# Kernel optimization log

Measured on AMD Instinct MI355X. Metric: run time of the kernel, lower is better.

The kernel has to match this reference:

```python
import jax, jax.numpy as jnp
import numpy as np

N_NODES = 50000
BN_EPS = 1e-5


def _gin_layer(x, src, dst, W1, b1, gamma, beta, W2, b2):
    # GINConv (eps=0): h = MLP(x + sum_{j->i} x_j)
    agg = jax.ops.segment_sum(x[src], dst, num_segments=N_NODES)  # [N, F]
    h = (x + agg) @ W1 + b1                                       # [N, H]
    # BatchNorm1d over node dim (training-mode batch statistics, biased var)
    mean = jnp.mean(h, axis=0)
    var = jnp.mean((h - mean) ** 2, axis=0)
    h = (h - mean) * jax.lax.rsqrt(var + BN_EPS) * gamma + beta
    h = jax.nn.relu(h)
    h = jax.nn.relu(h @ W2 + b2)
    return h


def setup_inputs() -> dict:
    key = jax.random.key(0)
    ks = jax.random.split(key, 16)
    F_in, H = 9, 256
    E = 800000
    x = jax.random.normal(ks[0], (N_NODES, F_in), dtype=jnp.float32)
    edge_index = jax.random.randint(ks[1], (2, E), 0, N_NODES, dtype=jnp.int64)

    def lin(k, fi, fo):
        s = 1.0 / np.sqrt(fi)
        kw, kb = jax.random.split(k)
        W = jax.random.uniform(kw, (fi, fo), jnp.float32, -s, s)
        b = jax.random.uniform(kb, (fo,), jnp.float32, -s, s)
        return W, b

    inp = {"x": x, "edge_index": edge_index}
    dims = [(F_in, H), (H, H), (H, H)]
    for i, (fi, fo) in enumerate(dims, start=1):
        W1, b1 = lin(ks[2 * i], fi, fo)
        W2, b2 = lin(ks[2 * i + 1], fo, fo)
        inp[f"W1_{i}"] = W1; inp[f"b1_{i}"] = b1
        inp[f"g_{i}"] = jnp.ones((fo,), jnp.float32)
        inp[f"be_{i}"] = jnp.zeros((fo,), jnp.float32)
        inp[f"W2_{i}"] = W2; inp[f"b2_{i}"] = b2
    return inp


def reference(x, edge_index,
              W1_1, b1_1, g_1, be_1, W2_1, b2_1,
              W1_2, b1_2, g_2, be_2, W2_2, b2_2,
              W1_3, b1_3, g_3, be_3, W2_3, b2_3):
    src, dst = edge_index[0], edge_index[1]
    h = _gin_layer(x, src, dst, W1_1, b1_1, g_1, be_1, W2_1, b2_1)
    h = jax.nn.relu(h)
    h = _gin_layer(h, src, dst, W1_2, b1_2, g_2, be_2, W2_2, b2_2)
    h = jax.nn.relu(h)
    h = _gin_layer(h, src, dst, W1_3, b1_3, g_3, be_3, W2_3, b2_3)
    h = jax.nn.relu(h)
    return jnp.sum(h, axis=0)  # [256]
```

## Files before the change

kernel.cpp:

```cpp
#include <hip/hip_runtime.h>

#define NN 50000
#define NE 800000
#define HD 256
#define BN_EPS 1e-5f

typedef __attribute__((ext_vector_type(8))) short bf16x8;
typedef __attribute__((ext_vector_type(8))) unsigned short ushort8;
typedef __attribute__((ext_vector_type(4))) float f32x4;

__device__ __forceinline__ float bf2f(unsigned short u) {
  union { unsigned int i; float f; } c; c.i = ((unsigned int)u) << 16; return c.f;
}
__device__ __forceinline__ unsigned short f2bf(float x) {
  union { float f; unsigned int i; } c; c.f = x;
  unsigned int r = (c.i + 0x7fffu + ((c.i >> 16) & 1u)) >> 16;
  return (unsigned short)r;
}

__global__ __launch_bounds__(1024) void k_zero(int* __restrict__ cursor, float* __restrict__ s_sum,
                                               float* __restrict__ s_sq, float* __restrict__ out) {
  int i = blockIdx.x * 1024 + threadIdx.x;
  if (i < NN) cursor[i] = 0;
  if (i < HD) { s_sum[i] = 0.f; s_sq[i] = 0.f; out[i] = 0.f; }
}

__global__ __launch_bounds__(256) void k_count(const int* __restrict__ dst, int* __restrict__ cnt) {
  int e = blockIdx.x * 256 + threadIdx.x;
  if (e < NE) atomicAdd(&cnt[dst[e]], 1);
}

__global__ __launch_bounds__(1024) void k_scan_a(const int* __restrict__ cnt,
                                                 int* __restrict__ rp, int* __restrict__ bsum) {
  __shared__ int wsum[16];
  int i = blockIdx.x * 1024 + threadIdx.x;
  int v = (i < NN) ? cnt[i] : 0;
  int lane = threadIdx.x & 63, wid = threadIdx.x >> 6;
  int s = v;
  #pragma unroll
  for (int off = 1; off < 64; off <<= 1) {
    int tv = __shfl_up(s, off);
    if (lane >= off) s += tv;
  }
  if (lane == 63) wsum[wid] = s;
  __syncthreads();
  if (wid == 0) {
    int ws = (lane < 16) ? wsum[lane] : 0;
    #pragma unroll
    for (int off = 1; off < 16; off <<= 1) {
      int tv = __shfl_up(ws, off);
      if (lane >= off) ws += tv;
    }
    if (lane < 16) wsum[lane] = ws;
  }
  __syncthreads();
  int excl = s - v + (wid > 0 ? wsum[wid - 1] : 0);
  if (i < NN) rp[i] = excl;
  if (threadIdx.x == 1023) bsum[blockIdx.x] = excl + v;
}

__global__ __launch_bounds__(1024) void k_scan_b(const int* __restrict__ bsum,
                                                 int* __restrict__ rp, int* __restrict__ cursor) {
  __shared__ int off_s;
  if (threadIdx.x < 64) {
    int v = ((int)threadIdx.x < (int)blockIdx.x && threadIdx.x < 49) ? bsum[threadIdx.x] : 0;
    #pragma unroll
    for (int o = 32; o > 0; o >>= 1) v += __shfl_xor(v, o);
    if (threadIdx.x == 0) off_s = v;
  }
  __syncthreads();
  int i = blockIdx.x * 1024 + threadIdx.x;
  if (i < NN) {
    int r = rp[i] + off_s;
    rp[i] = r;
    cursor[i] = r;
  }
  if (blockIdx.x == 0 && threadIdx.x == 0) rp[NN] = NE;
}

__global__ __launch_bounds__(256) void k_fill(const int* __restrict__ src, const int* __restrict__ dst,
                                              int* __restrict__ cursor, int* __restrict__ col) {
  int e = blockIdx.x * 256 + threadIdx.x;
  if (e < NE) {
    int p = atomicAdd(&cursor[dst[e]], 1);
    col[p] = src[e];
  }
}

__global__ __launch_bounds__(256) void k_prepW5(const float* __restrict__ Wa, const float* __restrict__ Wb,
    const float* __restrict__ Wc, const float* __restrict__ Wd, const float* __restrict__ We,
    unsigned short* __restrict__ out) {
  const float* W = (blockIdx.y == 0) ? Wa : (blockIdx.y == 1) ? Wb : (blockIdx.y == 2) ? Wc
                   : (blockIdx.y == 3) ? Wd : We;
  unsigned short* O = out + (size_t)blockIdx.y * HD * HD;
  int k = blockIdx.x, n = threadIdx.x;
  int nt = n >> 4, ks = k >> 5, lane = ((k >> 3) & 3) * 16 + (n & 15), j = k & 7;
  O[(size_t)((nt * 8 + ks) * 64 + lane) * 8 + j] = f2bf(W[k * 256 + n]);
}

__global__ __launch_bounds__(256) void k_agg9(const float* __restrict__ x,
    const int* __restrict__ rp, const int* __restrict__ col, float* __restrict__ u) {
  int i = blockIdx.x * 256 + threadIdx.x;
  if (i >= NN) return;
  float a[9];
  #pragma unroll
  for (int k = 0; k < 9; ++k) a[k] = x[(size_t)i * 9 + k];
  int e1 = rp[i + 1];
  for (int e = rp[i]; e < e1; ++e) {
    int nb = col[e];
    #pragma unroll
    for (int k = 0; k < 9; ++k) a[k] += x[(size_t)nb * 9 + k];
  }
  #pragma unroll
  for (int k = 0; k < 9; ++k) u[(size_t)i * 16 + k] = a[k];
}

__global__ __launch_bounds__(256) void k_l1gemm(const float* __restrict__ u,
    const float* __restrict__ W1, const float* __restrict__ b1,
    unsigned short* __restrict__ h, float* __restrict__ s_sum, float* __restrict__ s_sq) {
  __shared__ float Ws[9][256];
  int t = threadIdx.x;
  #pragma unroll
  for (int k = 0; k < 9; ++k) Ws[k][t] = W1[k * 256 + t];
  float bj = b1[t];
  __syncthreads();
  int r0 = blockIdx.x * 128;
  int r1 = min(r0 + 128, NN);
  float sum = 0.f, sq = 0.f;
  for (int r = r0; r < r1; ++r) {
    float acc = bj;
    #pragma unroll
    for (int k = 0; k < 9; ++k) acc = fmaf(u[(size_t)r * 16 + k], Ws[k][t], acc);
    h[(size_t)r * 256 + t] = f2bf(acc);
    sum += acc; sq += acc * acc;
  }
  atomicAdd(&s_sum[t], sum);
  atomicAdd(&s_sq[t], sq);
}

__global__ void k_finalize(float* __restrict__ s_sum, float* __restrict__ s_sq,
                           const float* __restrict__ g, const float* __restrict__ be,
                           float* __restrict__ scale, float* __restrict__ shift) {
  int j = threadIdx.x;
  float m = s_sum[j] / (float)NN;
  float v = s_sq[j] / (float)NN - m * m;
  v = fmaxf(v, 0.f);
  float sc = rsqrtf(v + BN_EPS) * g[j];
  scale[j] = sc;
  shift[j] = be[j] - m * sc;
  s_sum[j] = 0.f;
  s_sq[j] = 0.f;
}

__global__ __launch_bounds__(256) void k_bnapply(const unsigned short* __restrict__ h,
    const float* __restrict__ scale, const float* __restrict__ shift, unsigned short* __restrict__ a) {
  __shared__ float sc[256], sh[256];
  sc[threadIdx.x] = scale[threadIdx.x];
  sh[threadIdx.x] = shift[threadIdx.x];
  __syncthreads();
  const int total = NN * 32;
  for (int idx = blockIdx.x * 256 + threadIdx.x; idx < total; idx += gridDim.x * 256) {
    int c0 = (idx & 31) * 8;
    ushort8 v = *(const ushort8*)(h + (size_t)idx * 8);
    ushort8 o;
    #pragma unroll
    for (int j = 0; j < 8; ++j) {
      float f = bf2f(v[j]);
      f = fmaxf(fmaf(f, sc[c0 + j], sh[c0 + j]), 0.f);
      o[j] = f2bf(f);
    }
    *(ushort8*)(a + (size_t)idx * 8) = o;
  }
}

__global__ __launch_bounds__(256) void k_agg256(const unsigned short* __restrict__ f,
    const int* __restrict__ rp, const int* __restrict__ col, unsigned short* __restrict__ u) {
  int half = threadIdx.x >> 5;
  int lane32 = threadIdx.x & 31;
  int node = blockIdx.x * 8 + threadIdx.y * 2 + half;
  if (node >= NN) return;
  float acc[8];
  ushort8 v = *(const ushort8*)(f + (size_t)node * HD + lane32 * 8);
  #pragma unroll
  for (int j = 0; j < 8; ++j) acc[j] = bf2f(v[j]);
  int e0 = rp[node], e1 = rp[node + 1];
  int e = e0;
  for (; e + 1 < e1; e += 2) {
    int nb0 = col[e], nb1 = col[e + 1];
    ushort8 w0 = *(const ushort8*)(f + (size_t)nb0 * HD + lane32 * 8);
    ushort8 w1 = *(const ushort8*)(f + (size_t)nb1 * HD + lane32 * 8);
    #pragma unroll
    for (int j = 0; j < 8; ++j) acc[j] += bf2f(w0[j]) + bf2f(w1[j]);
  }
  if (e < e1) {
    int nb = col[e];
    ushort8 w = *(const ushort8*)(f + (size_t)nb * HD + lane32 * 8);
    #pragma unroll
    for (int j = 0; j < 8; ++j) acc[j] += bf2f(w[j]);
  }
  ushort8 o;
  #pragma unroll
  for (int j = 0; j < 8; ++j) o[j] = f2bf(acc[j]);
  *(ushort8*)(u + (size_t)node * HD + lane32 * 8) = o;
}

template<bool STATS, bool RELU, bool OUTSUM, bool WRITE>
__global__ __launch_bounds__(256, 3) void k_mfma_gemm(
    const unsigned short* __restrict__ A, const unsigned short* __restrict__ Bp,
    const float* __restrict__ bias, unsigned short* __restrict__ C,
    float* __restrict__ s_sum, float* __restrict__ s_sq, float* __restrict__ out)
{
  __shared__ unsigned short As[2][64 * 64];
  const int t = threadIdx.x;
  const int w = t >> 6;
  const int lane = t & 63;
  const int brow = blockIdx.x * 64;
  const bf16x8* Bf = (const bf16x8*)Bp;

  f32x4 zero; zero.x = zero.y = zero.z = zero.w = 0.f;
  f32x4 acc[4][4];
  #pragma unroll
  for (int i = 0; i < 4; ++i)
    #pragma unroll
    for (int j = 0; j < 4; ++j) acc[i][j] = zero;

  auto stage = [&](int buf, int kt) {
    #pragma unroll
    for (int hh = 0; hh < 2; ++hh) {
      int r0 = w * 16 + hh * 8;
      int row = r0 + (lane >> 3);
      int gp = (lane & 7) ^ (row & 7);
      int grow = brow + row; if (grow >= NN) grow = NN - 1;
      const unsigned short* gptr = A + (size_t)grow * HD + kt + gp * 8;
      __builtin_amdgcn_global_load_lds(
          (const __attribute__((address_space(1))) void*)gptr,
          (__attribute__((address_space(3))) void*)&As[buf][r0 * 64], 16, 0, 0);
    }
  };

  bf16x8 bcur[4], bnxt[4];
  #pragma unroll
  for (int ntl = 0; ntl < 4; ++ntl)
    bcur[ntl] = Bf[(size_t)((w * 4 + ntl) * 8 + 0) * 64 + lane];
  stage(0, 0);
  __syncthreads();

  #pragma unroll
  for (int step = 0; step < 8; ++step) {
    const int tt = step >> 1, s = step & 1;
    if (s == 0 && tt < 3) stage((tt + 1) & 1, (tt + 1) * 64);
    if (step < 7) {
      #pragma unroll
      for (int ntl = 0; ntl < 4; ++ntl)
        bnxt[ntl] = Bf[(size_t)((w * 4 + ntl) * 8 + step + 1) * 64 + lane];
    }
    bf16x8 afr[4];
    #pragma unroll
    for (int mt = 0; mt < 4; ++mt) {
      int row = mt * 16 + (lane & 15);
      int g = s * 4 + (lane >> 4);
      int gp = g ^ (row & 7);
      afr[mt] = *(const bf16x8*)&As[tt & 1][row * 64 + gp * 8];
    }
    #pragma unroll
    for (int mt = 0; mt < 4; ++mt)
      #pragma unroll
      for (int ntl = 0; ntl < 4; ++ntl)
        acc[mt][ntl] = __builtin_amdgcn_mfma_f32_16x16x32_bf16(
            afr[mt], bcur[ntl], acc[mt][ntl], 0, 0, 0);
    #pragma unroll
    for (int ntl = 0; ntl < 4; ++ntl) bcur[ntl] = bnxt[ntl];
    if (s == 1 && tt < 3) __syncthreads();
  }

  const int cl = lane & 15;
  const int rq = (lane >> 4) * 4;
  #pragma unroll
  for (int ntl = 0; ntl < 4; ++ntl) {
    const int cgl = w * 64 + ntl * 16 + cl;
    const float bv = bias[cgl];
    float s = 0.f, q = 0.f;
    #pragma unroll
    for (int mt = 0; mt < 4; ++mt) {
      #pragma unroll
      for (int i = 0; i < 4; ++i) {
        float v = acc[mt][ntl][i] + bv;
        if (RELU) v = fmaxf(v, 0.f);
        int grow = brow + mt * 16 + rq + i;
        bool valid = grow < NN;
        if (WRITE && valid) C[(size_t)grow * HD + cgl] = f2bf(v);
        if ((STATS || OUTSUM) && valid) { s += v; if (STATS) q += v * v; }
      }
    }
    if (STATS || OUTSUM) {
      s += __shfl_xor(s, 16); s += __shfl_xor(s, 32);
      if (STATS) { q += __shfl_xor(q, 16); q += __shfl_xor(q, 32); }
      if (lane < 16) {
        if (STATS) { atomicAdd(&s_sum[cgl], s); atomicAdd(&s_sq[cgl], q); }
        if (OUTSUM) atomicAdd(&out[cgl], s);
      }
    }
  }
}

extern "C" void kernel_launch(void* const* d_in, const int* in_sizes, int n_in,
                              void* d_out, int out_size, void* d_ws, size_t ws_size,
                              hipStream_t stream) {
  (void)in_sizes; (void)n_in; (void)out_size; (void)ws_size;
  const float* x  = (const float*)d_in[0];
  const int*  ei  = (const int*)d_in[1];
  const int*  src = ei;
  const int*  dst = ei + NE;
  const float* W1[3] = {(const float*)d_in[2],  (const float*)d_in[8],  (const float*)d_in[14]};
  const float* b1[3] = {(const float*)d_in[3],  (const float*)d_in[9],  (const float*)d_in[15]};
  const float* g_[3] = {(const float*)d_in[4],  (const float*)d_in[10], (const float*)d_in[16]};
  const float* be[3] = {(const float*)d_in[5],  (const float*)d_in[11], (const float*)d_in[17]};
  const float* W2[3] = {(const float*)d_in[6],  (const float*)d_in[12], (const float*)d_in[18]};
  const float* b2[3] = {(const float*)d_in[7],  (const float*)d_in[13], (const float*)d_in[19]};

  char* ws = (char*)d_ws;
  size_t o = 0;
  auto alloc = [&](size_t bytes) -> void* {
    void* p = ws + o;
    o += (bytes + 255) & ~(size_t)255;
    return p;
  };
  int*   rp     = (int*)alloc((size_t)(NN + 1) * 4);
  int*   cursor = (int*)alloc((size_t)NN * 4);
  int*   col    = (int*)alloc((size_t)NE * 4);
  int*   bsum   = (int*)alloc(64 * 4);
  float* u9     = (float*)alloc((size_t)NN * 16 * 4);
  unsigned short* ubf = (unsigned short*)alloc((size_t)NN * HD * 2);
  unsigned short* hbf = (unsigned short*)alloc((size_t)NN * HD * 2);
  unsigned short* abf = (unsigned short*)alloc((size_t)NN * HD * 2);
  unsigned short* fbf = (unsigned short*)alloc((size_t)NN * HD * 2);
  unsigned short* Wp  = (unsigned short*)alloc((size_t)5 * HD * HD * 2);
  float* s_sum  = (float*)alloc(HD * 4);
  float* s_sq   = (float*)alloc(HD * 4);
  float* scale  = (float*)alloc(HD * 4);
  float* shift  = (float*)alloc(HD * 4);
  float* out    = (float*)d_out;

  const int SCB = (NN + 1023) / 1024;

  k_zero<<<SCB, 1024, 0, stream>>>(cursor, s_sum, s_sq, out);
  k_count<<<(NE + 255) / 256, 256, 0, stream>>>(dst, cursor);
  k_scan_a<<<SCB, 1024, 0, stream>>>(cursor, rp, bsum);
  k_scan_b<<<SCB, 1024, 0, stream>>>(bsum, rp, cursor);
  k_fill<<<(NE + 255) / 256, 256, 0, stream>>>(src, dst, cursor, col);
  k_prepW5<<<dim3(256, 5), 256, 0, stream>>>(W2[0], W1[1], W2[1], W1[2], W2[2], Wp);

  unsigned short* WpA[5];
  for (int i = 0; i < 5; ++i) WpA[i] = Wp + (size_t)i * HD * HD;

  const int gemmGrid = (NN + 63) / 64;
  dim3 aGrid((NN + 7) / 8);
  dim3 aBlk(64, 4);

  k_agg9<<<(NN + 255) / 256, 256, 0, stream>>>(x, rp, col, u9);
  k_l1gemm<<<(NN + 127) / 128, 256, 0, stream>>>(u9, W1[0], b1[0], hbf, s_sum, s_sq);
  k_finalize<<<1, HD, 0, stream>>>(s_sum, s_sq, g_[0], be[0], scale, shift);
  k_bnapply<<<2048, 256, 0, stream>>>(hbf, scale, shift, abf);
  k_mfma_gemm<false, true, false, true><<<gemmGrid, 256, 0, stream>>>(
      abf, WpA[0], b2[0], fbf, nullptr, nullptr, nullptr);

  k_agg256<<<aGrid, aBlk, 0, stream>>>(fbf, rp, col, ubf);
  k_mfma_gemm<true, false, false, true><<<gemmGrid, 256, 0, stream>>>(
      ubf, WpA[1], b1[1], hbf, s_sum, s_sq, nullptr);
  k_finalize<<<1, HD, 0, stream>>>(s_sum, s_sq, g_[1], be[1], scale, shift);
  k_bnapply<<<2048, 256, 0, stream>>>(hbf, scale, shift, abf);
  k_mfma_gemm<false, true, false, true><<<gemmGrid, 256, 0, stream>>>(
      abf, WpA[2], b2[1], fbf, nullptr, nullptr, nullptr);

  k_agg256<<<aGrid, aBlk, 0, stream>>>(fbf, rp, col, ubf);
  k_mfma_gemm<true, false, false, true><<<gemmGrid, 256, 0, stream>>>(
      ubf, WpA[3], b1[2], hbf, s_sum, s_sq, nullptr);
  k_finalize<<<1, HD, 0, stream>>>(s_sum, s_sq, g_[2], be[2], scale, shift);
  k_bnapply<<<2048, 256, 0, stream>>>(hbf, scale, shift, abf);
  k_mfma_gemm<false, true, true, false><<<gemmGrid, 256, 0, stream>>>(
      abf, WpA[4], b2[2], nullptr, nullptr, nullptr, out);
}
```

Baseline: 469.0 us.

## Prefetch full A tile into LDS up front and deepen B register pipeline

```diff
diff --git a/kernel.cpp b/kernel.cpp
--- a/kernel.cpp
+++ b/kernel.cpp
@@ -185,14 +185,17 @@
   for (int j = 0; j < 8; ++j) acc[j] = bf2f(v[j]);
   int e0 = rp[node], e1 = rp[node + 1];
   int e = e0;
-  for (; e + 1 < e1; e += 2) {
-    int nb0 = col[e], nb1 = col[e + 1];
+  for (; e + 3 < e1; e += 4) {
+    int nb0 = col[e], nb1 = col[e + 1], nb2 = col[e + 2], nb3 = col[e + 3];
     ushort8 w0 = *(const ushort8*)(f + (size_t)nb0 * HD + lane32 * 8);
     ushort8 w1 = *(const ushort8*)(f + (size_t)nb1 * HD + lane32 * 8);
-    #pragma unroll
-    for (int j = 0; j < 8; ++j) acc[j] += bf2f(w0[j]) + bf2f(w1[j]);
-  }
-  if (e < e1) {
+    ushort8 w2 = *(const ushort8*)(f + (size_t)nb2 * HD + lane32 * 8);
+    ushort8 w3 = *(const ushort8*)(f + (size_t)nb3 * HD + lane32 * 8);
+    #pragma unroll
+    for (int j = 0; j < 8; ++j)
+      acc[j] += (bf2f(w0[j]) + bf2f(w1[j])) + (bf2f(w2[j]) + bf2f(w3[j]));
+  }
+  for (; e < e1; ++e) {
     int nb = col[e];
     ushort8 w = *(const ushort8*)(f + (size_t)nb * HD + lane32 * 8);
     #pragma unroll
@@ -210,67 +213,66 @@
     const float* __restrict__ bias, unsigned short* __restrict__ C,
     float* __restrict__ s_sum, float* __restrict__ s_sq, float* __restrict__ out)
 {
-  __shared__ unsigned short As[2][64 * 64];
+  __shared__ unsigned short As[4][64 * 64];
   const int t = threadIdx.x;
   const int w = t >> 6;
   const int lane = t & 63;
   const int brow = blockIdx.x * 64;
   const bf16x8* Bf = (const bf16x8*)Bp;
 
-  f32x4 zero; zero.x = zero.y = zero.z = zero.w = 0.f;
-  f32x4 acc[4][4];
-  #pragma unroll
-  for (int i = 0; i < 4; ++i)
-    #pragma unroll
-    for (int j = 0; j < 4; ++j) acc[i][j] = zero;
-
-  auto stage = [&](int buf, int kt) {
+  #pragma unroll
+  for (int tt = 0; tt < 4; ++tt) {
     #pragma unroll
     for (int hh = 0; hh < 2; ++hh) {
       int r0 = w * 16 + hh * 8;
       int row = r0 + (lane >> 3);
       int gp = (lane & 7) ^ (row & 7);
       int grow = brow + row; if (grow >= NN) grow = NN - 1;
-      const unsigned short* gptr = A + (size_t)grow * HD + kt + gp * 8;
+      const unsigned short* gptr = A + (size_t)grow * HD + tt * 64 + gp * 8;
       __builtin_amdgcn_global_load_lds(
           (const __attribute__((address_space(1))) void*)gptr,
-          (__attribute__((address_space(3))) void*)&As[buf][r0 * 64], 16, 0, 0);
-    }
-  };
-
-  bf16x8 bcur[4], bnxt[4];
-  #pragma unroll
-  for (int ntl = 0; ntl < 4; ++ntl)
-    bcur[ntl] = Bf[(size_t)((w * 4 + ntl) * 8 + 0) * 64 + lane];
-  stage(0, 0);
-  __syncthreads();
+          (__attribute__((address_space(3))) void*)&As[tt][r0 * 64], 16, 0, 0);
+    }
+  }
+
+  bf16x8 bfr[3][4];
+  #pragma unroll
+  for (int p = 0; p < 3; ++p)
+    #pragma unroll
+    for (int ntl = 0; ntl < 4; ++ntl)
+      bfr[p][ntl] = Bf[(size_t)((w * 4 + ntl) * 8 + p) * 64 + lane];
+
+  f32x4 zero; zero.x = zero.y = zero.z = zero.w = 0.f;
+  f32x4 acc[4][4];
+  #pragma unroll
+  for (int i = 0; i < 4; ++i)
+    #pragma unroll
+    for (int j = 0; j < 4; ++j) acc[i][j] = zero;
 
   #pragma unroll
   for (int step = 0; step < 8; ++step) {
     const int tt = step >> 1, s = step & 1;
-    if (s == 0 && tt < 3) stage((tt + 1) & 1, (tt + 1) * 64);
-    if (step < 7) {
-      #pragma unroll
-      for (int ntl = 0; ntl < 4; ++ntl)
-        bnxt[ntl] = Bf[(size_t)((w * 4 + ntl) * 8 + step + 1) * 64 + lane];
-    }
+    if (s == 0) __syncthreads();
+    const int cur = step % 3;
     bf16x8 afr[4];
     #pragma unroll
     for (int mt = 0; mt < 4; ++mt) {
       int row = mt * 16 + (lane & 15);
       int g = s * 4 + (lane >> 4);
       int gp = g ^ (row & 7);
-      afr[mt] = *(const bf16x8*)&As[tt & 1][row * 64 + gp * 8];
+      afr[mt] = *(const bf16x8*)&As[tt][row * 64 + gp * 8];
     }
     #pragma unroll
     for (int mt = 0; mt < 4; ++mt)
       #pragma unroll
       for (int ntl = 0; ntl < 4; ++ntl)
         acc[mt][ntl] = __builtin_amdgcn_mfma_f32_16x16x32_bf16(
-            afr[mt], bcur[ntl], acc[mt][ntl], 0, 0, 0);
-    #pragma unroll
-    for (int ntl = 0; ntl < 4; ++ntl) bcur[ntl] = bnxt[ntl];
-    if (s == 1 && tt < 3) __syncthreads();
+            afr[mt], bfr[cur][ntl], acc[mt][ntl], 0, 0, 0);
+    if (step < 5) {
+      #pragma unroll
+      for (int ntl = 0; ntl < 4; ++ntl)
+        bfr[cur][ntl] = Bf[(size_t)((w * 4 + ntl) * 8 + step + 3) * 64 + lane];
+    }
   }
 
   const int cl = lane & 15;
```

Result: no change. 470.1 us (+0.2%).
